# Performance work log

Hardware: AMD Instinct MI355X
Metric: run time of the kernel (lower is better)

## Reference

```python
import jax, jax.numpy as jnp
import numpy as np

N_NODES = 100000
N_EDGES = 3200000
IN_DIM = 128
HID = 64
OUT_DIM = 128
N_GRAPHS = 8


def _gcn_conv(x, W, b, src, dst, w, n):
    # GCNConv (PyG default): add self-loops (weight 1), symmetric normalization
    loop = jnp.arange(n)
    src2 = jnp.concatenate([src, loop])
    dst2 = jnp.concatenate([dst, loop])
    w2 = jnp.concatenate([w, jnp.ones((n,), x.dtype)])
    deg = jax.ops.segment_sum(w2, dst2, num_segments=n)
    dinv = jnp.where(deg > 0, jax.lax.rsqrt(deg), 0.0)
    norm = dinv[src2] * w2 * dinv[dst2]            # [E+N]
    h = x @ W                                      # transform before gather
    msg = h[src2] * norm[:, None]                  # gather + scale
    out = jax.ops.segment_sum(msg, dst2, num_segments=n)  # scatter-add
    return out + b


def setup_inputs() -> dict:
    key = jax.random.key(0)
    ks = jax.random.split(key, 10)
    x = jax.random.normal(ks[0], (N_NODES, IN_DIM), dtype=jnp.float32)
    edge_index = jax.random.randint(ks[1], (2, N_EDGES), 0, N_NODES, dtype=jnp.int64)
    edge_weight = jax.random.uniform(ks[2], (N_EDGES,), dtype=jnp.float32)
    batch = jnp.sort(jax.random.randint(ks[3], (N_NODES,), 0, N_GRAPHS, dtype=jnp.int64))
    # params (glorot-ish scale)
    W1 = jax.random.normal(ks[4], (IN_DIM, HID), dtype=jnp.float32) / np.sqrt(IN_DIM)
    b1 = jnp.zeros((HID,), jnp.float32)
    W2 = jax.random.normal(ks[5], (HID, HID), dtype=jnp.float32) / np.sqrt(HID)
    b2 = jnp.zeros((HID,), jnp.float32)
    Wfc = jax.random.normal(ks[6], (HID, OUT_DIM), dtype=jnp.float32) / np.sqrt(HID)
    bfc = jnp.zeros((OUT_DIM,), jnp.float32)
    return {"x": x, "edge_index": edge_index, "edge_weight": edge_weight,
            "batch": batch, "W1": W1, "b1": b1, "W2": W2, "b2": b2,
            "Wfc": Wfc, "bfc": bfc}


def reference(x, edge_index, edge_weight, batch, W1, b1, W2, b2, Wfc, bfc):
    src, dst = edge_index[0], edge_index[1]
    n = x.shape[0]
    h = _gcn_conv(x, W1, b1, src, dst, edge_weight, n)
    h = jax.nn.relu(h)
    h = _gcn_conv(h, W2, b2, src, dst, edge_weight, n)
    # global_mean_pool over batch ids
    sums = jax.ops.segment_sum(h, batch, num_segments=N_GRAPHS)
    cnts = jax.ops.segment_sum(jnp.ones((n,), h.dtype), batch, num_segments=N_GRAPHS)
    pooled = sums / jnp.maximum(cnts, 1.0)[:, None]
    return pooled @ Wfc + bfc
```

## Files before the change

### kernel.cpp

```cpp
#include <hip/hip_runtime.h>

#define IN_DIM 128
#define HID 64
#define OUT_DIM 128
#define NGRAPH 8

#define CHUNK 4096
#define BSH 7
#define BSZ 128
#define MAXB 800

typedef unsigned long long u64;
typedef unsigned int u32;
typedef __attribute__((ext_vector_type(8))) short short8;
typedef __attribute__((ext_vector_type(4))) float f32x4;

__device__ inline short bf16b(float f) {
    u32 u = __float_as_uint(f);
    return (short)((u + 0x7FFFu + ((u >> 16) & 1u)) >> 16);
}
__device__ inline u32 pack_bf16(float a, float b) {
    u32 ua = (__float_as_uint(a) + 0x8000u) >> 16;
    u32 ub = (__float_as_uint(b) + 0x8000u) & 0xFFFF0000u;
    return ua | ub;
}
__device__ inline float bf16_lo(u32 v) { return __uint_as_float(v << 16); }
__device__ inline float bf16_hi(u32 v) { return __uint_as_float(v & 0xFFFF0000u); }

__global__ __launch_bounds__(256) void bhist_kernel(const int* __restrict__ dst,
                                                    u32* __restrict__ hist,
                                                    int E, int nchunk, int nbuck) {
    __shared__ u32 h[MAXB];
    for (int i = threadIdx.x; i < nbuck; i += 256) h[i] = 0;
    __syncthreads();
    int c = blockIdx.x;
    int beg = c * CHUNK, end = min(beg + CHUNK, E);
    for (int i = beg + threadIdx.x; i < end; i += 256)
        atomicAdd(&h[dst[i] >> BSH], 1u);
    __syncthreads();
    for (int b = threadIdx.x; b < nbuck; b += 256)
        hist[(size_t)b * nchunk + c] = h[b];
}

__global__ __launch_bounds__(512) void scanS1(u32* __restrict__ hist, u32* __restrict__ tot,
                                              int nchunk, int nbuck) {
    __shared__ u32 sm[1024];
    int b = blockIdx.x;
    int i0 = threadIdx.x, i1 = threadIdx.x + 512;
    u32 v0 = (i0 < nchunk) ? hist[(size_t)b * nchunk + i0] : 0;
    u32 v1 = (i1 < nchunk) ? hist[(size_t)b * nchunk + i1] : 0;
    sm[i0] = v0; sm[i1] = v1;
    __syncthreads();
    for (int off = 1; off < 1024; off <<= 1) {
        u32 t0 = (i0 >= off) ? sm[i0 - off] : 0;
        u32 t1 = (i1 >= off) ? sm[i1 - off] : 0;
        __syncthreads();
        sm[i0] += t0; sm[i1] += t1;
        __syncthreads();
    }
    if (i0 < nchunk) hist[(size_t)b * nchunk + i0] = sm[i0] - v0;
    if (i1 < nchunk) hist[(size_t)b * nchunk + i1] = sm[i1] - v1;
    if (threadIdx.x == 511) tot[b] = sm[1023];
}

__global__ __launch_bounds__(1024) void scanS2(const u32* __restrict__ tot,
                                               u32* __restrict__ base, int nbuck) {
    __shared__ u32 sm[2048];
    int i0 = threadIdx.x, i1 = threadIdx.x + 1024;
    u32 v0 = (i0 < nbuck) ? tot[i0] : 0;
    u32 v1 = (i1 < nbuck) ? tot[i1] : 0;
    sm[i0] = v0; sm[i1] = v1;
    __syncthreads();
    for (int off = 1; off < 2048; off <<= 1) {
        u32 t0 = (i0 >= off) ? sm[i0 - off] : 0;
        u32 t1 = (i1 >= off) ? sm[i1 - off] : 0;
        __syncthreads();
        sm[i0] += t0; sm[i1] += t1;
        __syncthreads();
    }
    if (i0 <= nbuck) base[i0] = sm[i0] - v0;
    if (i1 <= nbuck) base[i1] = sm[i1] - v1;
}

__global__ __launch_bounds__(256) void bin_kernel(const int* __restrict__ src,
                                                  const int* __restrict__ dst,
                                                  const float* __restrict__ ew,
                                                  const u32* __restrict__ offs,
                                                  const u32* __restrict__ base,
                                                  int2* __restrict__ bse,
                                                  int E, int nchunk, int nbuck) {
    __shared__ u32 lcnt[MAXB];
    __shared__ u32 lpos[MAXB];
    __shared__ u32 gbase[MAXB];
    __shared__ u32 part[256];
    __shared__ int2 buf[CHUNK];
    __shared__ unsigned short bb[CHUNK];

    int c = blockIdx.x;
    int tid = threadIdx.x;
    int beg = c * CHUNK, end = min(beg + CHUNK, E);
    for (int b = tid; b < nbuck; b += 256) lcnt[b] = 0;
    __syncthreads();
    for (int i = beg + tid; i < end; i += 256)
        atomicAdd(&lcnt[dst[i] >> BSH], 1u);
    __syncthreads();
    int SEG = (nbuck + 255) >> 8;
    u32 s = 0;
    for (int j = 0; j < SEG; ++j) {
        int b = tid * SEG + j;
        if (b < nbuck) s += lcnt[b];
    }
    part[tid] = s;
    __syncthreads();
    for (int off = 1; off < 256; off <<= 1) {
        u32 t = (tid >= off) ? part[tid - off] : 0;
        __syncthreads();
        part[tid] += t;
        __syncthreads();
    }
    u32 run = part[tid] - s;
    for (int j = 0; j < SEG; ++j) {
        int b = tid * SEG + j;
        if (b < nbuck) { u32 cv = lcnt[b]; lpos[b] = run; run += cv; }
    }
    __syncthreads();
    for (int b = tid; b < nbuck; b += 256) {
        lcnt[b] = lpos[b];
        gbase[b] = base[b] + offs[(size_t)b * nchunk + c];
    }
    __syncthreads();
    for (int i = beg + tid; i < end; i += 256) {
        int d = dst[i];
        int b = d >> BSH;
        u32 p = atomicAdd(&lcnt[b], 1u);
        buf[p] = make_int2(src[i] | ((d & (BSZ - 1)) << 17), __float_as_int(ew[i]));
        bb[p] = (unsigned short)b;
    }
    __syncthreads();
    int tot = end - beg;
    for (int j = tid; j < tot; j += 256) {
        int b = bb[j];
        bse[gbase[b] + j - lpos[b]] = buf[j];
    }
}

__global__ __launch_bounds__(256) void csr_kernel(const int2* __restrict__ bse,
                                                  const u32* __restrict__ base,
                                                  int* __restrict__ row_ptr,
                                                  float* __restrict__ dinv,
                                                  int2* __restrict__ edges, int N) {
    __shared__ u32 cnt[BSZ];
    __shared__ u32 wd[BSZ];
    __shared__ u32 rp[BSZ];
    int b = blockIdx.x;
    int tid = threadIdx.x;
    int beg = base[b], end = base[b + 1];
    if (tid < BSZ) { cnt[tid] = 0; wd[tid] = 0; }
    __syncthreads();
    for (int i = beg + tid; i < end; i += 256) {
        int2 e = bse[i];
        int dl = (e.x >> 17) & (BSZ - 1);
        atomicAdd(&cnt[dl], 1u);
        atomicAdd(&wd[dl], (u32)__float2int_rn(__int_as_float(e.y) * 1048576.0f));
    }
    __syncthreads();
    u32 v = 0;
    if (tid < BSZ) { v = cnt[tid]; rp[tid] = v; }
    __syncthreads();
    for (int off = 1; off < BSZ; off <<= 1) {
        u32 t = 0;
        if (tid < BSZ && tid >= off) t = rp[tid - off];
        __syncthreads();
        if (tid < BSZ) rp[tid] += t;
        __syncthreads();
    }
    if (tid < BSZ) {
        int node = b * BSZ + tid;
        u32 excl = rp[tid] - v;
        if (node <= N) row_ptr[node] = beg + (int)excl;
        if (node < N)
            dinv[node] = rsqrtf((float)wd[tid] * (1.0f / 1048576.0f) + 1.0f);
    }
    __syncthreads();
    if (tid < BSZ) cnt[tid] = rp[tid] - v;
    __syncthreads();
    for (int i = beg + tid; i < end; i += 256) {
        int2 e = bse[i];
        int dl = (e.x >> 17) & (BSZ - 1);
        u32 r = atomicAdd(&cnt[dl], 1u);
        edges[beg + r] = make_int2(e.x & 0x1FFFF, e.y);
    }
}

__global__ __launch_bounds__(256) void gemm1_kernel(const float* __restrict__ x,
                                                    const float* __restrict__ W1,
                                                    const float* __restrict__ dinv,
                                                    u32* __restrict__ hb, int N) {
    int wave = threadIdx.x >> 6, lane = threadIdx.x & 63;
    int col = lane & 15, kg = lane >> 4;
    int rowbase = blockIdx.x * 64 + wave * 16;

    short8 bW[4][4];
#pragma unroll
    for (int ks = 0; ks < 4; ++ks)
#pragma unroll
        for (int nt = 0; nt < 4; ++nt) {
            const float* wp = W1 + (size_t)(ks * 32 + kg * 8) * HID + nt * 16 + col;
            short8 f;
#pragma unroll
            for (int j = 0; j < 8; ++j) f[j] = bf16b(wp[j * HID]);
            bW[ks][nt] = f;
        }

    f32x4 acc[4];
#pragma unroll
    for (int nt = 0; nt < 4; ++nt) acc[nt] = (f32x4){0.f, 0.f, 0.f, 0.f};

    int arow = rowbase + col;
    if (arow >= N) arow = N - 1;
    const float4* xr = reinterpret_cast<const float4*>(x + (size_t)arow * IN_DIM);
#pragma unroll
    for (int ks = 0; ks < 4; ++ks) {
        float4 xa = xr[ks * 8 + kg * 2];
        float4 xb = xr[ks * 8 + kg * 2 + 1];
        short8 a;
        a[0] = bf16b(xa.x); a[1] = bf16b(xa.y); a[2] = bf16b(xa.z); a[3] = bf16b(xa.w);
        a[4] = bf16b(xb.x); a[5] = bf16b(xb.y); a[6] = bf16b(xb.z); a[7] = bf16b(xb.w);
#pragma unroll
        for (int nt = 0; nt < 4; ++nt)
            acc[nt] = __builtin_amdgcn_mfma_f32_16x16x32_bf16(a, bW[ks][nt], acc[nt], 0, 0, 0);
    }

#pragma unroll
    for (int r = 0; r < 4; ++r) {
        int row = rowbase + kg * 4 + r;
        if (row < N) {
            float di = dinv[row];
            hb[(size_t)row * 32 + col]      = pack_bf16(acc[0][r] * di, acc[2][r] * di);
            hb[(size_t)row * 32 + col + 16] = pack_bf16(acc[1][r] * di, acc[3][r] * di);
        }
    }
}

__global__ void agg_kernel(const int* __restrict__ row_ptr, const int2* __restrict__ edges,
                           const float* __restrict__ dinv, const u32* __restrict__ hb,
                           u32* __restrict__ aggb, int N) {
    int gid = blockIdx.x * blockDim.x + threadIdx.x;
    int node = gid >> 6, lane = gid & 63;
    if (node >= N) return;
    int half = lane >> 5, l = lane & 31;
    int beg = row_ptr[node], end = row_ptr[node + 1];
    int mid = beg + ((end - beg + 1) >> 1);
    int lo = half ? mid : beg;
    int hi = half ? end : mid;
    float ax = 0.f, ay = 0.f;
    if (half == 0) {
        u32 hv = hb[(size_t)node * 32 + l];
        ax = bf16_lo(hv);
        ay = bf16_hi(hv);
    }
    int i = lo;
    for (; i + 8 <= hi; i += 8) {
        int2 e0 = edges[i+0], e1 = edges[i+1], e2 = edges[i+2], e3 = edges[i+3];
        int2 e4 = edges[i+4], e5 = edges[i+5], e6 = edges[i+6], e7 = edges[i+7];
        u32 h0 = hb[(size_t)e0.x * 32 + l], h1 = hb[(size_t)e1.x * 32 + l];
        u32 h2 = hb[(size_t)e2.x * 32 + l], h3 = hb[(size_t)e3.x * 32 + l];
        u32 h4 = hb[(size_t)e4.x * 32 + l], h5 = hb[(size_t)e5.x * 32 + l];
        u32 h6 = hb[(size_t)e6.x * 32 + l], h7 = hb[(size_t)e7.x * 32 + l];
        float c0 = __int_as_float(e0.y), c1 = __int_as_float(e1.y);
        float c2 = __int_as_float(e2.y), c3 = __int_as_float(e3.y);
        float c4 = __int_as_float(e4.y), c5 = __int_as_float(e5.y);
        float c6 = __int_as_float(e6.y), c7 = __int_as_float(e7.y);
        ax += c0 * bf16_lo(h0); ay += c0 * bf16_hi(h0);
        ax += c1 * bf16_lo(h1); ay += c1 * bf16_hi(h1);
        ax += c2 * bf16_lo(h2); ay += c2 * bf16_hi(h2);
        ax += c3 * bf16_lo(h3); ay += c3 * bf16_hi(h3);
        ax += c4 * bf16_lo(h4); ay += c4 * bf16_hi(h4);
        ax += c5 * bf16_lo(h5); ay += c5 * bf16_hi(h5);
        ax += c6 * bf16_lo(h6); ay += c6 * bf16_hi(h6);
        ax += c7 * bf16_lo(h7); ay += c7 * bf16_hi(h7);
    }
    if (i < hi) {
        int2 e[8];
#pragma unroll
        for (int k = 0; k < 8; ++k) {
            int j = i + k;
            e[k] = edges[j < hi ? j : i];
            if (j >= hi) e[k].y = 0;
        }
        u32 hh[8];
#pragma unroll
        for (int k = 0; k < 8; ++k) hh[k] = hb[(size_t)e[k].x * 32 + l];
#pragma unroll
        for (int k = 0; k < 8; ++k) {
            float c = __int_as_float(e[k].y);
            ax += c * bf16_lo(hh[k]);
            ay += c * bf16_hi(hh[k]);
        }
    }
    ax += __shfl_xor(ax, 32);
    ay += __shfl_xor(ay, 32);
    float di = dinv[node];
    if (lane < 32) aggb[(size_t)node * 32 + l] = pack_bf16(di * ax, di * ay);
}

__global__ __launch_bounds__(256) void gemm2_kernel(const u32* __restrict__ aggb,
                                                    const float* __restrict__ b1,
                                                    const float* __restrict__ W2,
                                                    const float* __restrict__ dinv,
                                                    u32* __restrict__ hb, int N) {
    int wave = threadIdx.x >> 6, lane = threadIdx.x & 63;
    int col = lane & 15, kg = lane >> 4;
    int rowbase = blockIdx.x * 64 + wave * 16;

    short8 bW[2][4];
#pragma unroll
    for (int ks = 0; ks < 2; ++ks)
#pragma unroll
        for (int nt = 0; nt < 4; ++nt) {
            const float* wp = W2 + (size_t)(ks * 32 + kg * 8) * HID + nt * 16 + col;
            short8 f;
#pragma unroll
            for (int j = 0; j < 8; ++j) f[j] = bf16b(wp[j * HID]);
            bW[ks][nt] = f;
        }

    f32x4 acc[4];
#pragma unroll
    for (int nt = 0; nt < 4; ++nt) acc[nt] = (f32x4){0.f, 0.f, 0.f, 0.f};

    int arow = rowbase + col;
    if (arow >= N) arow = N - 1;
    const u32* ar = aggb + (size_t)arow * 32 + kg * 8;
    u32 w[8];
#pragma unroll
    for (int j = 0; j < 8; ++j) w[j] = ar[j];
#pragma unroll
    for (int ks = 0; ks < 2; ++ks) {
        short8 a;
#pragma unroll
        for (int j = 0; j < 8; ++j) {
            float f = ks ? bf16_hi(w[j]) : bf16_lo(w[j]);
            a[j] = bf16b(fmaxf(f + b1[ks * 32 + kg * 8 + j], 0.f));
        }
#pragma unroll
        for (int nt = 0; nt < 4; ++nt)
            acc[nt] = __builtin_amdgcn_mfma_f32_16x16x32_bf16(a, bW[ks][nt], acc[nt], 0, 0, 0);
    }

#pragma unroll
    for (int r = 0; r < 4; ++r) {
        int row = rowbase + kg * 4 + r;
        if (row < N) {
            float di = dinv[row];
            hb[(size_t)row * 32 + col]      = pack_bf16(acc[0][r] * di, acc[2][r] * di);
            hb[(size_t)row * 32 + col + 16] = pack_bf16(acc[1][r] * di, acc[3][r] * di);
        }
    }
}

__global__ void pool_kernel(const u32* __restrict__ aggb, const int* __restrict__ batch,
                            float* __restrict__ pooled, float* __restrict__ cnt,
                            int N, int chunk) {
    int wid = (blockIdx.x * blockDim.x + threadIdx.x) >> 6;
    int lane = threadIdx.x & 63;
    int w = lane & 31, hi = lane >> 5;
    int feat = w + hi * 32;
    int start = wid * chunk;
    if (start >= N) return;
    int end = min(start + chunk, N);
    float acc = 0.f, fc = 0.f;
    int cur = batch[start];
    for (int n = start; n < end; ++n) {
        int g = batch[n];
        if (g != cur) {
            atomicAdd(&pooled[cur * HID + feat], acc);
            if (lane == 0) atomicAdd(&cnt[cur], fc);
            cur = g; acc = 0.f; fc = 0.f;
        }
        u32 hv = aggb[(size_t)n * 32 + w];
        acc += hi ? bf16_hi(hv) : bf16_lo(hv);
        fc += 1.f;
    }
    atomicAdd(&pooled[cur * HID + feat], acc);
    if (lane == 0) atomicAdd(&cnt[cur], fc);
}

__global__ void final_kernel(const float* __restrict__ pooled, const float* __restrict__ cnt,
                             const float* __restrict__ b2, const float* __restrict__ Wfc,
                             const float* __restrict__ bfc, float* __restrict__ out) {
    int idx = blockIdx.x * blockDim.x + threadIdx.x;
    if (idx >= NGRAPH * OUT_DIM) return;
    int g = idx >> 7, o = idx & 127;
    float inv = 1.0f / fmaxf(cnt[g], 1.0f);
    float acc = 0.f;
#pragma unroll
    for (int k = 0; k < HID; ++k)
        acc += (pooled[g * HID + k] * inv + b2[k]) * Wfc[k * OUT_DIM + o];
    out[idx] = acc + bfc[o];
}

extern "C" void kernel_launch(void* const* d_in, const int* in_sizes, int n_in,
                              void* d_out, int out_size, void* d_ws, size_t ws_size,
                              hipStream_t stream) {
    const float* x    = (const float*)d_in[0];
    const int*   ei   = (const int*)d_in[1];
    const float* ew   = (const float*)d_in[2];
    const int*   bat  = (const int*)d_in[3];
    const float* W1   = (const float*)d_in[4];
    const float* b1   = (const float*)d_in[5];
    const float* W2   = (const float*)d_in[6];
    const float* b2   = (const float*)d_in[7];
    const float* Wfc  = (const float*)d_in[8];
    const float* bfc  = (const float*)d_in[9];
    float* out = (float*)d_out;

    const int N = in_sizes[0] / IN_DIM;
    const int E = in_sizes[2];
    const int* src = ei;
    const int* dst = ei + E;

    const int nbuck  = (N + BSZ - 1) >> BSH;
    const int nchunk = (E + CHUNK - 1) / CHUNK;

    char* ws = (char*)d_ws;
    size_t off = 0;
    auto alloc = [&](size_t bytes) {
        char* p = ws + off;
        off += (bytes + 255) / 256 * 256;
        return p;
    };
    u32*   hist    = (u32*)  alloc((size_t)nbuck * nchunk * 4);
    u32*   tot     = (u32*)  alloc(2048 * 4);
    u32*   base    = (u32*)  alloc(2048 * 4);
    int*   row_ptr = (int*)  alloc((size_t)(N + 1) * 4);
    float* dinv    = (float*)alloc((size_t)N * 4);
    float* pooled  = (float*)alloc((NGRAPH * HID + NGRAPH) * 4);
    float* cnt     = pooled + NGRAPH * HID;
    int2*  bse     = (int2*) alloc((size_t)E * 8);
    int2*  edges   = (int2*) alloc((size_t)E * 8);
    u32*   hb      = (u32*)  alloc((size_t)N * 32 * 4);
    u32*   aggb    = (u32*)  alloc((size_t)N * 32 * 4);

    hipMemsetAsync(pooled, 0, (NGRAPH * HID + NGRAPH) * 4, stream);

    bhist_kernel<<<nchunk, 256, 0, stream>>>(dst, hist, E, nchunk, nbuck);
    scanS1<<<nbuck, 512, 0, stream>>>(hist, tot, nchunk, nbuck);
    scanS2<<<1, 1024, 0, stream>>>(tot, base, nbuck);
    bin_kernel<<<nchunk, 256, 0, stream>>>(src, dst, ew, hist, base, bse, E, nchunk, nbuck);
    csr_kernel<<<nbuck, 256, 0, stream>>>(bse, base, row_ptr, dinv, edges, N);

    int gemmBlocks = (N + 63) / 64;
    int rowBlocks = (int)(((size_t)N * 64 + 255) / 256);

    gemm1_kernel<<<gemmBlocks, 256, 0, stream>>>(x, W1, dinv, hb, N);
    agg_kernel<<<rowBlocks, 256, 0, stream>>>(row_ptr, edges, dinv, hb, aggb, N);

    gemm2_kernel<<<gemmBlocks, 256, 0, stream>>>(aggb, b1, W2, dinv, hb, N);
    agg_kernel<<<rowBlocks, 256, 0, stream>>>(row_ptr, edges, dinv, hb, aggb, N);

    const int POOL_WAVES = 1024;
    int chunk = (N + POOL_WAVES - 1) / POOL_WAVES;
    pool_kernel<<<POOL_WAVES / 4, 256, 0, stream>>>(aggb, bat, pooled, cnt, N, chunk);

    final_kernel<<<(NGRAPH * OUT_DIM + 255) / 256, 256, 0, stream>>>(pooled, cnt, b2, Wfc, bfc, out);
}
```

Measured before the change: 306.7 us.

## Widen agg gathers to 8-byte loads and fuse scan and pool/final kernels

Aggregation now has each 16-lane group handle a separate edge stream with 8-byte loads per lane. This gives four edges in flight per wave, and partial sums are reduced by shuffles. The two-level scan and the pool/final stages are merged into single kernels using a last-block atomic counter, which removes two launches. The cost is extra atomics and fences, plus serial tail work in one block.

```diff
diff --git a/kernel.cpp b/kernel.cpp
--- a/kernel.cpp
+++ b/kernel.cpp
@@ -42,9 +42,13 @@
         hist[(size_t)b * nchunk + c] = h[b];
 }
 
-__global__ __launch_bounds__(512) void scanS1(u32* __restrict__ hist, u32* __restrict__ tot,
-                                              int nchunk, int nbuck) {
+__global__ __launch_bounds__(512) void scan_kernel(u32* __restrict__ hist,
+                                                   u32* __restrict__ tot,
+                                                   u32* __restrict__ base,
+                                                   u32* __restrict__ sync,
+                                                   int nchunk, int nbuck) {
     __shared__ u32 sm[1024];
+    __shared__ u32 lastFlag;
     int b = blockIdx.x;
     int i0 = threadIdx.x, i1 = threadIdx.x + 512;
     u32 v0 = (i0 < nchunk) ? hist[(size_t)b * nchunk + i0] : 0;
@@ -61,25 +65,28 @@
     if (i0 < nchunk) hist[(size_t)b * nchunk + i0] = sm[i0] - v0;
     if (i1 < nchunk) hist[(size_t)b * nchunk + i1] = sm[i1] - v1;
     if (threadIdx.x == 511) tot[b] = sm[1023];
-}
-
-__global__ __launch_bounds__(1024) void scanS2(const u32* __restrict__ tot,
-                                               u32* __restrict__ base, int nbuck) {
-    __shared__ u32 sm[2048];
-    int i0 = threadIdx.x, i1 = threadIdx.x + 1024;
-    u32 v0 = (i0 < nbuck) ? tot[i0] : 0;
-    u32 v1 = (i1 < nbuck) ? tot[i1] : 0;
-    sm[i0] = v0; sm[i1] = v1;
-    __syncthreads();
-    for (int off = 1; off < 2048; off <<= 1) {
-        u32 t0 = (i0 >= off) ? sm[i0 - off] : 0;
-        u32 t1 = (i1 >= off) ? sm[i1 - off] : 0;
-        __syncthreads();
-        sm[i0] += t0; sm[i1] += t1;
-        __syncthreads();
-    }
-    if (i0 <= nbuck) base[i0] = sm[i0] - v0;
-    if (i1 <= nbuck) base[i1] = sm[i1] - v1;
+    __threadfence();
+    __syncthreads();
+    if (threadIdx.x == 0)
+        lastFlag = (atomicAdd(sync, 1u) == (u32)(gridDim.x - 1)) ? 1u : 0u;
+    __syncthreads();
+    if (lastFlag) {
+        __threadfence();
+        u32 w0 = (i0 < nbuck) ? tot[i0] : 0;
+        u32 w1 = (i1 < nbuck) ? tot[i1] : 0;
+        __syncthreads();
+        sm[i0] = w0; sm[i1] = w1;
+        __syncthreads();
+        for (int off = 1; off < 1024; off <<= 1) {
+            u32 t0 = (i0 >= off) ? sm[i0 - off] : 0;
+            u32 t1 = (i1 >= off) ? sm[i1 - off] : 0;
+            __syncthreads();
+            sm[i0] += t0; sm[i1] += t1;
+            __syncthreads();
+        }
+        if (i0 <= nbuck) base[i0] = sm[i0] - w0;
+        if (i1 <= nbuck) base[i1] = sm[i1] - w1;
+    }
 }
 
 __global__ __launch_bounds__(256) void bin_kernel(const int* __restrict__ src,
@@ -243,65 +250,60 @@
 }
 
 __global__ void agg_kernel(const int* __restrict__ row_ptr, const int2* __restrict__ edges,
-                           const float* __restrict__ dinv, const u32* __restrict__ hb,
-                           u32* __restrict__ aggb, int N) {
+                           const float* __restrict__ dinv, const int2* __restrict__ hb2,
+                           int2* __restrict__ aggb2, int N) {
     int gid = blockIdx.x * blockDim.x + threadIdx.x;
     int node = gid >> 6, lane = gid & 63;
     if (node >= N) return;
-    int half = lane >> 5, l = lane & 31;
+    int q = lane >> 4, s = lane & 15;
     int beg = row_ptr[node], end = row_ptr[node + 1];
-    int mid = beg + ((end - beg + 1) >> 1);
-    int lo = half ? mid : beg;
-    int hi = half ? end : mid;
-    float ax = 0.f, ay = 0.f;
-    if (half == 0) {
-        u32 hv = hb[(size_t)node * 32 + l];
-        ax = bf16_lo(hv);
-        ay = bf16_hi(hv);
-    }
-    int i = lo;
-    for (; i + 8 <= hi; i += 8) {
-        int2 e0 = edges[i+0], e1 = edges[i+1], e2 = edges[i+2], e3 = edges[i+3];
-        int2 e4 = edges[i+4], e5 = edges[i+5], e6 = edges[i+6], e7 = edges[i+7];
-        u32 h0 = hb[(size_t)e0.x * 32 + l], h1 = hb[(size_t)e1.x * 32 + l];
-        u32 h2 = hb[(size_t)e2.x * 32 + l], h3 = hb[(size_t)e3.x * 32 + l];
-        u32 h4 = hb[(size_t)e4.x * 32 + l], h5 = hb[(size_t)e5.x * 32 + l];
-        u32 h6 = hb[(size_t)e6.x * 32 + l], h7 = hb[(size_t)e7.x * 32 + l];
-        float c0 = __int_as_float(e0.y), c1 = __int_as_float(e1.y);
-        float c2 = __int_as_float(e2.y), c3 = __int_as_float(e3.y);
-        float c4 = __int_as_float(e4.y), c5 = __int_as_float(e5.y);
-        float c6 = __int_as_float(e6.y), c7 = __int_as_float(e7.y);
-        ax += c0 * bf16_lo(h0); ay += c0 * bf16_hi(h0);
-        ax += c1 * bf16_lo(h1); ay += c1 * bf16_hi(h1);
-        ax += c2 * bf16_lo(h2); ay += c2 * bf16_hi(h2);
-        ax += c3 * bf16_lo(h3); ay += c3 * bf16_hi(h3);
-        ax += c4 * bf16_lo(h4); ay += c4 * bf16_hi(h4);
-        ax += c5 * bf16_lo(h5); ay += c5 * bf16_hi(h5);
-        ax += c6 * bf16_lo(h6); ay += c6 * bf16_hi(h6);
-        ax += c7 * bf16_lo(h7); ay += c7 * bf16_hi(h7);
-    }
-    if (i < hi) {
+    float a0 = 0.f, a1 = 0.f, a2 = 0.f, a3 = 0.f;
+    int i = beg + q;
+    for (; i + 28 < end; i += 32) {
         int2 e[8];
 #pragma unroll
-        for (int k = 0; k < 8; ++k) {
-            int j = i + k;
-            e[k] = edges[j < hi ? j : i];
-            if (j >= hi) e[k].y = 0;
-        }
-        u32 hh[8];
-#pragma unroll
-        for (int k = 0; k < 8; ++k) hh[k] = hb[(size_t)e[k].x * 32 + l];
+        for (int k = 0; k < 8; ++k) e[k] = edges[i + 4 * k];
+        int2 w[8];
+#pragma unroll
+        for (int k = 0; k < 8; ++k) w[k] = hb2[(size_t)e[k].x * 16 + s];
 #pragma unroll
         for (int k = 0; k < 8; ++k) {
             float c = __int_as_float(e[k].y);
-            ax += c * bf16_lo(hh[k]);
-            ay += c * bf16_hi(hh[k]);
-        }
-    }
-    ax += __shfl_xor(ax, 32);
-    ay += __shfl_xor(ay, 32);
-    float di = dinv[node];
-    if (lane < 32) aggb[(size_t)node * 32 + l] = pack_bf16(di * ax, di * ay);
+            a0 += c * bf16_lo(w[k].x); a1 += c * bf16_hi(w[k].x);
+            a2 += c * bf16_lo(w[k].y); a3 += c * bf16_hi(w[k].y);
+        }
+    }
+    if (i < end) {
+        int2 e[8];
+#pragma unroll
+        for (int k = 0; k < 8; ++k) {
+            int j = i + 4 * k;
+            bool vld = j < end;
+            e[k] = edges[vld ? j : beg];
+            if (!vld) e[k].y = 0;
+        }
+        int2 w[8];
+#pragma unroll
+        for (int k = 0; k < 8; ++k) w[k] = hb2[(size_t)e[k].x * 16 + s];
+#pragma unroll
+        for (int k = 0; k < 8; ++k) {
+            float c = __int_as_float(e[k].y);
+            a0 += c * bf16_lo(w[k].x); a1 += c * bf16_hi(w[k].x);
+            a2 += c * bf16_lo(w[k].y); a3 += c * bf16_hi(w[k].y);
+        }
+    }
+    a0 += __shfl_xor(a0, 16); a0 += __shfl_xor(a0, 32);
+    a1 += __shfl_xor(a1, 16); a1 += __shfl_xor(a1, 32);
+    a2 += __shfl_xor(a2, 16); a2 += __shfl_xor(a2, 32);
+    a3 += __shfl_xor(a3, 16); a3 += __shfl_xor(a3, 32);
+    if (lane < 16) {
+        int2 wv = hb2[(size_t)node * 16 + s];
+        a0 += bf16_lo(wv.x); a1 += bf16_hi(wv.x);
+        a2 += bf16_lo(wv.y); a3 += bf16_hi(wv.y);
+        float di = dinv[node];
+        aggb2[(size_t)node * 16 + s] = make_int2(pack_bf16(di * a0, di * a1),
+                                                 pack_bf16(di * a2, di * a3));
+    }
 }
 
 __global__ __launch_bounds__(256) void gemm2_kernel(const u32* __restrict__ aggb,
@@ -359,45 +361,57 @@
     }
 }
 
-__global__ void pool_kernel(const u32* __restrict__ aggb, const int* __restrict__ batch,
-                            float* __restrict__ pooled, float* __restrict__ cnt,
-                            int N, int chunk) {
+__global__ __launch_bounds__(256) void pool_kernel(const u32* __restrict__ aggb,
+                                                   const int* __restrict__ batch,
+                                                   float* __restrict__ pooled,
+                                                   float* __restrict__ cnt,
+                                                   u32* __restrict__ sync,
+                                                   const float* __restrict__ b2,
+                                                   const float* __restrict__ Wfc,
+                                                   const float* __restrict__ bfc,
+                                                   float* __restrict__ out,
+                                                   int N, int chunk) {
+    __shared__ u32 lastFlag;
     int wid = (blockIdx.x * blockDim.x + threadIdx.x) >> 6;
     int lane = threadIdx.x & 63;
     int w = lane & 31, hi = lane >> 5;
     int feat = w + hi * 32;
     int start = wid * chunk;
-    if (start >= N) return;
-    int end = min(start + chunk, N);
-    float acc = 0.f, fc = 0.f;
-    int cur = batch[start];
-    for (int n = start; n < end; ++n) {
-        int g = batch[n];
-        if (g != cur) {
-            atomicAdd(&pooled[cur * HID + feat], acc);
-            if (lane == 0) atomicAdd(&cnt[cur], fc);
-            cur = g; acc = 0.f; fc = 0.f;
-        }
-        u32 hv = aggb[(size_t)n * 32 + w];
-        acc += hi ? bf16_hi(hv) : bf16_lo(hv);
-        fc += 1.f;
-    }
-    atomicAdd(&pooled[cur * HID + feat], acc);
-    if (lane == 0) atomicAdd(&cnt[cur], fc);
-}
-
-__global__ void final_kernel(const float* __restrict__ pooled, const float* __restrict__ cnt,
-                             const float* __restrict__ b2, const float* __restrict__ Wfc,
-                             const float* __restrict__ bfc, float* __restrict__ out) {
-    int idx = blockIdx.x * blockDim.x + threadIdx.x;
-    if (idx >= NGRAPH * OUT_DIM) return;
-    int g = idx >> 7, o = idx & 127;
-    float inv = 1.0f / fmaxf(cnt[g], 1.0f);
-    float acc = 0.f;
-#pragma unroll
-    for (int k = 0; k < HID; ++k)
-        acc += (pooled[g * HID + k] * inv + b2[k]) * Wfc[k * OUT_DIM + o];
-    out[idx] = acc + bfc[o];
+    if (start < N) {
+        int end = min(start + chunk, N);
+        float acc = 0.f, fc = 0.f;
+        int cur = batch[start];
+        for (int n = start; n < end; ++n) {
+            int g = batch[n];
+            if (g != cur) {
+                atomicAdd(&pooled[cur * HID + feat], acc);
+                if (lane == 0) atomicAdd(&cnt[cur], fc);
+                cur = g; acc = 0.f; fc = 0.f;
+            }
+            u32 hv = aggb[(size_t)n * 32 + w];
+            acc += hi ? bf16_hi(hv) : bf16_lo(hv);
+            fc += 1.f;
+        }
+        atomicAdd(&pooled[cur * HID + feat], acc);
+        if (lane == 0) atomicAdd(&cnt[cur], fc);
+    }
+    __threadfence();
+    __syncthreads();
+    if (threadIdx.x == 0)
+        lastFlag = (atomicAdd(sync, 1u) == (u32)(gridDim.x - 1)) ? 1u : 0u;
+    __syncthreads();
+    if (lastFlag) {
+        __threadfence();
+        for (int idx = threadIdx.x; idx < NGRAPH * OUT_DIM; idx += 256) {
+            int g = idx >> 7, o = idx & 127;
+            float inv = 1.0f / fmaxf(cnt[g], 1.0f);
+            float acc = 0.f;
+#pragma unroll
+            for (int k = 0; k < HID; ++k)
+                acc += (pooled[g * HID + k] * inv + b2[k]) * Wfc[k * OUT_DIM + o];
+            out[idx] = acc + bfc[o];
+        }
+    }
 }
 
 extern "C" void kernel_launch(void* const* d_in, const int* in_sizes, int n_in,
@@ -435,18 +449,19 @@
     u32*   base    = (u32*)  alloc(2048 * 4);
     int*   row_ptr = (int*)  alloc((size_t)(N + 1) * 4);
     float* dinv    = (float*)alloc((size_t)N * 4);
-    float* pooled  = (float*)alloc((NGRAPH * HID + NGRAPH) * 4);
+    float* pooled  = (float*)alloc((NGRAPH * HID + NGRAPH + 2) * 4);
     float* cnt     = pooled + NGRAPH * HID;
+    u32*   syncA   = (u32*)(cnt + NGRAPH);
+    u32*   syncB   = syncA + 1;
     int2*  bse     = (int2*) alloc((size_t)E * 8);
     int2*  edges   = (int2*) alloc((size_t)E * 8);
     u32*   hb      = (u32*)  alloc((size_t)N * 32 * 4);
     u32*   aggb    = (u32*)  alloc((size_t)N * 32 * 4);
 
-    hipMemsetAsync(pooled, 0, (NGRAPH * HID + NGRAPH) * 4, stream);
+    hipMemsetAsync(pooled, 0, (NGRAPH * HID + NGRAPH + 2) * 4, stream);
 
     bhist_kernel<<<nchunk, 256, 0, stream>>>(dst, hist, E, nchunk, nbuck);
-    scanS1<<<nbuck, 512, 0, stream>>>(hist, tot, nchunk, nbuck);
-    scanS2<<<1, 1024, 0, stream>>>(tot, base, nbuck);
+    scan_kernel<<<nbuck, 512, 0, stream>>>(hist, tot, base, syncA, nchunk, nbuck);
     bin_kernel<<<nchunk, 256, 0, stream>>>(src, dst, ew, hist, base, bse, E, nchunk, nbuck);
     csr_kernel<<<nbuck, 256, 0, stream>>>(bse, base, row_ptr, dinv, edges, N);
 
@@ -454,14 +469,15 @@
     int rowBlocks = (int)(((size_t)N * 64 + 255) / 256);
 
     gemm1_kernel<<<gemmBlocks, 256, 0, stream>>>(x, W1, dinv, hb, N);
-    agg_kernel<<<rowBlocks, 256, 0, stream>>>(row_ptr, edges, dinv, hb, aggb, N);
+    agg_kernel<<<rowBlocks, 256, 0, stream>>>(row_ptr, edges, dinv, (const int2*)hb,
+                                              (int2*)aggb, N);
 
     gemm2_kernel<<<gemmBlocks, 256, 0, stream>>>(aggb, b1, W2, dinv, hb, N);
-    agg_kernel<<<rowBlocks, 256, 0, stream>>>(row_ptr, edges, dinv, hb, aggb, N);
+    agg_kernel<<<rowBlocks, 256, 0, stream>>>(row_ptr, edges, dinv, (const int2*)hb,
+                                              (int2*)aggb, N);
 
     const int POOL_WAVES = 1024;
     int chunk = (N + POOL_WAVES - 1) / POOL_WAVES;
-    pool_kernel<<<POOL_WAVES / 4, 256, 0, stream>>>(aggb, bat, pooled, cnt, N, chunk);
-
-    final_kernel<<<(NGRAPH * OUT_DIM + 255) / 256, 256, 0, stream>>>(pooled, cnt, b2, Wfc, bfc, out);
-}
+    pool_kernel<<<POOL_WAVES / 4, 256, 0, stream>>>(aggb, bat, pooled, cnt, syncB,
+                                                    b2, Wfc, bfc, out, N, chunk);
+}
```

After: 465.8 us. 1.52x slower.
